# Performance work log

Hardware: AMD Instinct MI355X
Metric: run time of the kernel (lower is better)

Reference implementation:

```python
import jax, jax.numpy as jnp
import numpy as np

B, H, S, D = 4, 16, 2048, 64
SCALE_FACTOR = 8.0  # forward arg; module multiplies qk by 1/scale_factor = 0.125 = 1/sqrt(D)
# dropout_p is an undefined global in the source module; treated as 0 (identity)
# for a deterministic reference.

def setup_inputs() -> dict:
    key0 = jax.random.key(0)
    kq, kk, kv = jax.random.split(key0, 3)
    query = jax.random.normal(kq, (B, H, S, D), dtype=jnp.float32)
    key = jax.random.normal(kk, (B, H, S, D), dtype=jnp.float32)
    value = jax.random.normal(kv, (B, H, S, D), dtype=jnp.float32)
    return {"query": query, "key": key, "value": value}

def reference(query, key, value):
    inv_scale = 1.0 / SCALE_FACTOR
    # [B,H,S,S] attention scores (the module materializes this full matrix)
    qk = jnp.einsum('bhqd,bhkd->bhqk', query, key) * inv_scale
    probs = jax.nn.softmax(qk, axis=-1)
    # dropout is identity (p effectively 0 / eval-mode deterministic baseline)
    out = jnp.einsum('bhqk,bhkd->bhqd', probs, value)
    return out
```

## Files before the change

kernel.cpp:

```cpp
#include <hip/hip_runtime.h>
#include <hip/hip_bf16.h>

#define SEQ 2048
#define DIMH 64
#define KB 64
#define NT (SEQ / KB)

typedef __attribute__((ext_vector_type(8))) short bf16x8;
typedef __attribute__((ext_vector_type(4))) float f32x4;

extern "C" __device__ float __ocml_native_exp2_f32(float);
#define EXP2(x) __ocml_native_exp2_f32(x)

__device__ inline unsigned short f2bf(float f) {
    union { __bf16 h; unsigned short u; } c;
    c.h = (__bf16)f;
    return c.u;
}
__device__ inline unsigned pack2(float a, float b) {
    return (unsigned)f2bf(a) | ((unsigned)f2bf(b) << 16);
}

__device__ inline int swz(int row, int col) {
    int g = (((row & 7) ^ ((row >> 3) & 7)) << 3);
    return row * 64 + (col ^ g);
}

__device__ inline void perm32swap(unsigned &a, unsigned &b) {
    asm("v_permlane32_swap_b32 %0, %1" : "+v"(a), "+v"(b));
}
__device__ inline void perm16swap(unsigned &a, unsigned &b) {
    asm("v_permlane16_swap_b32 %0, %1" : "+v"(a), "+v"(b));
}

__global__ __launch_bounds__(256, 4) void fattn(
    const float* __restrict__ Q, const float* __restrict__ K,
    const float* __restrict__ V, float* __restrict__ O)
{
    __shared__ __align__(16) unsigned short Ksh[KB * DIMH];
    __shared__ __align__(16) unsigned short Vt[DIMH * KB];

    const int tid  = threadIdx.x;
    const int lane = tid & 63;
    const int wv   = tid >> 6;
    const int bh   = blockIdx.x >> 4;
    const int qt   = blockIdx.x & 15;

    const int l15 = lane & 15;
    const int lg  = lane >> 4;

    const float* qh = Q + (size_t)bh * SEQ * DIMH;
    const float* kh = K + (size_t)bh * SEQ * DIMH;
    const float* vh = V + (size_t)bh * SEQ * DIMH;
    float*       oh = O + (size_t)bh * SEQ * DIMH;

    const int q0 = qt * 128 + wv * 32;

    int koff[4][2];
    #pragma unroll
    for (int n = 0; n < 4; ++n)
        #pragma unroll
        for (int ks = 0; ks < 2; ++ks)
            koff[n][ks] = swz(n * 16 + l15, ks * 32 + lg * 8);

    const int c4 = (tid & 15) * 4;
    const int rK = tid >> 4;
    int kstoff[4], vstoff[4];
    #pragma unroll
    for (int rr = 0; rr < 4; ++rr) kstoff[rr] = swz(rr * 16 + rK, c4);
    #pragma unroll
    for (int j = 0; j < 4; ++j) vstoff[j] = swz(c4 + j, rK * 4);

    const float QS = 0.180336880111120f;
    bf16x8 qf[2][2];
    #pragma unroll
    for (int h = 0; h < 2; ++h)
        #pragma unroll
        for (int ks = 0; ks < 2; ++ks) {
            const float* src = qh + (size_t)(q0 + h * 16 + l15) * DIMH + ks * 32 + lg * 8;
            f32x4 a = *reinterpret_cast<const f32x4*>(src);
            f32x4 b = *reinterpret_cast<const f32x4*>(src + 4);
            bf16x8 vq;
            #pragma unroll
            for (int j = 0; j < 4; ++j) {
                vq[j]     = (short)f2bf(a[j] * QS);
                vq[j + 4] = (short)f2bf(b[j] * QS);
            }
            qf[h][ks] = vq;
        }

    bf16x8 ones;
    #pragma unroll
    for (int j = 0; j < 8; ++j) ones[j] = (short)0x3F80;

    f32x4 oacc[2][4];
    #pragma unroll
    for (int h = 0; h < 2; ++h)
        #pragma unroll
        for (int d = 0; d < 4; ++d) oacc[h][d] = (f32x4){0.f, 0.f, 0.f, 0.f};
    f32x4 lacc[2] = {{0.f,0.f,0.f,0.f}, {0.f,0.f,0.f,0.f}};

    for (int kt = 0; kt < NT; ++kt) {
        __syncthreads();

        #pragma unroll
        for (int rr = 0; rr < 4; ++rr) {
            const f32x4 k4 = *reinterpret_cast<const f32x4*>(
                kh + (size_t)(kt * KB + rr * 16 + rK) * DIMH + c4);
            uint2 kk;
            kk.x = pack2(k4[0], k4[1]);
            kk.y = pack2(k4[2], k4[3]);
            *reinterpret_cast<uint2*>(&Ksh[kstoff[rr]]) = kk;
        }
        {
            f32x4 v4[4];
            #pragma unroll
            for (int i = 0; i < 4; ++i)
                v4[i] = *reinterpret_cast<const f32x4*>(
                    vh + (size_t)(kt * KB + rK * 4 + i) * DIMH + c4);
            #pragma unroll
            for (int j = 0; j < 4; ++j) {
                uint2 w;
                w.x = pack2(v4[0][j], v4[1][j]);
                w.y = pack2(v4[2][j], v4[3][j]);
                *reinterpret_cast<uint2*>(&Vt[vstoff[j]]) = w;
            }
        }
        __syncthreads();

        __builtin_amdgcn_s_setprio(1);

        unsigned u[2][8];
        #pragma unroll
        for (int n = 0; n < 4; ++n) {
            bf16x8 kf0 = *reinterpret_cast<const bf16x8*>(&Ksh[koff[n][0]]);
            bf16x8 kf1 = *reinterpret_cast<const bf16x8*>(&Ksh[koff[n][1]]);
            #pragma unroll
            for (int h = 0; h < 2; ++h) {
                f32x4 a = {0.f, 0.f, 0.f, 0.f};
                a = __builtin_amdgcn_mfma_f32_16x16x32_bf16(kf0, qf[h][0], a, 0, 0, 0);
                a = __builtin_amdgcn_mfma_f32_16x16x32_bf16(kf1, qf[h][1], a, 0, 0, 0);
                u[h][2 * n]     = pack2(EXP2(a[0]), EXP2(a[1]));
                u[h][2 * n + 1] = pack2(EXP2(a[2]), EXP2(a[3]));
            }
        }

        bf16x8 pa[2][2];
        #pragma unroll
        for (int h = 0; h < 2; ++h)
            #pragma unroll
            for (int ks = 0; ks < 2; ++ks) {
                unsigned a0 = u[h][4 * ks + 0], b0 = u[h][4 * ks + 2];
                unsigned a1 = u[h][4 * ks + 1], b1 = u[h][4 * ks + 3];
                perm32swap(a0, b0); perm16swap(a0, b0);
                perm32swap(a1, b1); perm16swap(a1, b1);
                union { unsigned w[4]; bf16x8 v; } pu;
                pu.w[0] = a0; pu.w[1] = a1; pu.w[2] = b0; pu.w[3] = b1;
                pa[h][ks] = pu.v;
            }

        #pragma unroll
        for (int h = 0; h < 2; ++h) {
            lacc[h] = __builtin_amdgcn_mfma_f32_16x16x32_bf16(pa[h][0], ones, lacc[h], 0, 0, 0);
            lacc[h] = __builtin_amdgcn_mfma_f32_16x16x32_bf16(pa[h][1], ones, lacc[h], 0, 0, 0);
        }

        #pragma unroll
        for (int d = 0; d < 4; ++d) {
            bf16x8 vb0 = *reinterpret_cast<const bf16x8*>(&Vt[koff[d][0]]);
            bf16x8 vb1 = *reinterpret_cast<const bf16x8*>(&Vt[koff[d][1]]);
            #pragma unroll
            for (int h = 0; h < 2; ++h) {
                oacc[h][d] = __builtin_amdgcn_mfma_f32_16x16x32_bf16(pa[h][0], vb0, oacc[h][d], 0, 0, 0);
                oacc[h][d] = __builtin_amdgcn_mfma_f32_16x16x32_bf16(pa[h][1], vb1, oacc[h][d], 0, 0, 0);
            }
        }

        __builtin_amdgcn_s_setprio(0);
    }

    #pragma unroll
    for (int h = 0; h < 2; ++h)
        #pragma unroll
        for (int r = 0; r < 4; ++r) {
            float inv = 1.0f / lacc[h][r];
            float* dst = oh + (size_t)(q0 + h * 16 + lg * 4 + r) * DIMH;
            #pragma unroll
            for (int d = 0; d < 4; ++d)
                dst[d * 16 + l15] = oacc[h][d][r] * inv;
        }
}

extern "C" void kernel_launch(void* const* d_in, const int* in_sizes, int n_in,
                              void* d_out, int out_size, void* d_ws, size_t ws_size,
                              hipStream_t stream) {
    const float* q = (const float*)d_in[0];
    const float* k = (const float*)d_in[1];
    const float* v = (const float*)d_in[2];
    float* out = (float*)d_out;
    dim3 grid(64 * (SEQ / 128));
    dim3 block(256);
    fattn<<<grid, block, 0, stream>>>(q, k, v, out);
}
```

Baseline: 109.7 us.

## Double-buffer K/V tiles in LDS with register prefetch and remap block order

Splits the K and V shared-memory tiles into two buffers. The next tile's global loads are issued into registers before the P·V MFMAs of the current tile, then converted and stored into the other buffer afterwards, leaving one barrier per iteration instead of two. It also remaps block indices so that consecutive blocks map to different heads, changing L2 locality. The cost is 16 more KB of LDS and 32 extra VGPRs of prefetch registers, which may reduce occupancy under launch_bounds(256,4).

```diff
diff --git a/kernel.cpp b/kernel.cpp
--- a/kernel.cpp
+++ b/kernel.cpp
@@ -37,14 +37,17 @@
     const float* __restrict__ Q, const float* __restrict__ K,
     const float* __restrict__ V, float* __restrict__ O)
 {
-    __shared__ __align__(16) unsigned short Ksh[KB * DIMH];
-    __shared__ __align__(16) unsigned short Vt[DIMH * KB];
+    __shared__ __align__(16) unsigned short Ksh[2][KB * DIMH];
+    __shared__ __align__(16) unsigned short Vt[2][KB * DIMH];
 
     const int tid  = threadIdx.x;
     const int lane = tid & 63;
     const int wv   = tid >> 6;
-    const int bh   = blockIdx.x >> 4;
-    const int qt   = blockIdx.x & 15;
+
+    const int bid = blockIdx.x;
+    const int swb = (bid & 7) * 128 + (bid >> 3);
+    const int bh  = swb >> 4;
+    const int qt  = swb & 15;
 
     const int l15 = lane & 15;
     const int lg  = lane >> 4;
@@ -100,41 +103,43 @@
         for (int d = 0; d < 4; ++d) oacc[h][d] = (f32x4){0.f, 0.f, 0.f, 0.f};
     f32x4 lacc[2] = {{0.f,0.f,0.f,0.f}, {0.f,0.f,0.f,0.f}};
 
-    for (int kt = 0; kt < NT; ++kt) {
-        __syncthreads();
-
+    {
         #pragma unroll
         for (int rr = 0; rr < 4; ++rr) {
             const f32x4 k4 = *reinterpret_cast<const f32x4*>(
-                kh + (size_t)(kt * KB + rr * 16 + rK) * DIMH + c4);
+                kh + (size_t)(rr * 16 + rK) * DIMH + c4);
             uint2 kk;
             kk.x = pack2(k4[0], k4[1]);
             kk.y = pack2(k4[2], k4[3]);
-            *reinterpret_cast<uint2*>(&Ksh[kstoff[rr]]) = kk;
-        }
-        {
-            f32x4 v4[4];
-            #pragma unroll
-            for (int i = 0; i < 4; ++i)
-                v4[i] = *reinterpret_cast<const f32x4*>(
-                    vh + (size_t)(kt * KB + rK * 4 + i) * DIMH + c4);
-            #pragma unroll
-            for (int j = 0; j < 4; ++j) {
-                uint2 w;
-                w.x = pack2(v4[0][j], v4[1][j]);
-                w.y = pack2(v4[2][j], v4[3][j]);
-                *reinterpret_cast<uint2*>(&Vt[vstoff[j]]) = w;
-            }
-        }
-        __syncthreads();
+            *reinterpret_cast<uint2*>(&Ksh[0][kstoff[rr]]) = kk;
+        }
+        f32x4 v4[4];
+        #pragma unroll
+        for (int i = 0; i < 4; ++i)
+            v4[i] = *reinterpret_cast<const f32x4*>(
+                vh + (size_t)(rK * 4 + i) * DIMH + c4);
+        #pragma unroll
+        for (int j = 0; j < 4; ++j) {
+            uint2 w;
+            w.x = pack2(v4[0][j], v4[1][j]);
+            w.y = pack2(v4[2][j], v4[3][j]);
+            *reinterpret_cast<uint2*>(&Vt[0][vstoff[j]]) = w;
+        }
+    }
+    __syncthreads();
+
+    for (int kt = 0; kt < NT; ++kt) {
+        const int cur = kt & 1;
+        const unsigned short* Kb = Ksh[cur];
+        const unsigned short* Vb = Vt[cur];
 
         __builtin_amdgcn_s_setprio(1);
 
         unsigned u[2][8];
         #pragma unroll
         for (int n = 0; n < 4; ++n) {
-            bf16x8 kf0 = *reinterpret_cast<const bf16x8*>(&Ksh[koff[n][0]]);
-            bf16x8 kf1 = *reinterpret_cast<const bf16x8*>(&Ksh[koff[n][1]]);
+            bf16x8 kf0 = *reinterpret_cast<const bf16x8*>(&Kb[koff[n][0]]);
+            bf16x8 kf1 = *reinterpret_cast<const bf16x8*>(&Kb[koff[n][1]]);
             #pragma unroll
             for (int h = 0; h < 2; ++h) {
                 f32x4 a = {0.f, 0.f, 0.f, 0.f};
@@ -159,6 +164,20 @@
                 pa[h][ks] = pu.v;
             }
 
+        f32x4 kreg[4], vreg[4];
+        const bool pf = (kt + 1 < NT);
+        if (pf) {
+            const size_t tb = (size_t)(kt + 1) * KB;
+            #pragma unroll
+            for (int rr = 0; rr < 4; ++rr)
+                kreg[rr] = *reinterpret_cast<const f32x4*>(
+                    kh + (tb + rr * 16 + rK) * DIMH + c4);
+            #pragma unroll
+            for (int i = 0; i < 4; ++i)
+                vreg[i] = *reinterpret_cast<const f32x4*>(
+                    vh + (tb + rK * 4 + i) * DIMH + c4);
+        }
+
         #pragma unroll
         for (int h = 0; h < 2; ++h) {
             lacc[h] = __builtin_amdgcn_mfma_f32_16x16x32_bf16(pa[h][0], ones, lacc[h], 0, 0, 0);
@@ -167,8 +186,8 @@
 
         #pragma unroll
         for (int d = 0; d < 4; ++d) {
-            bf16x8 vb0 = *reinterpret_cast<const bf16x8*>(&Vt[koff[d][0]]);
-            bf16x8 vb1 = *reinterpret_cast<const bf16x8*>(&Vt[koff[d][1]]);
+            bf16x8 vb0 = *reinterpret_cast<const bf16x8*>(&Vb[koff[d][0]]);
+            bf16x8 vb1 = *reinterpret_cast<const bf16x8*>(&Vb[koff[d][1]]);
             #pragma unroll
             for (int h = 0; h < 2; ++h) {
                 oacc[h][d] = __builtin_amdgcn_mfma_f32_16x16x32_bf16(pa[h][0], vb0, oacc[h][d], 0, 0, 0);
@@ -177,6 +196,27 @@
         }
 
         __builtin_amdgcn_s_setprio(0);
+
+        if (pf) {
+            const int nxt = cur ^ 1;
+            #pragma unroll
+            for (int rr = 0; rr < 4; ++rr) {
+                uint2 kk;
+                kk.x = pack2(kreg[rr][0], kreg[rr][1]);
+                kk.y = pack2(kreg[rr][2], kreg[rr][3]);
+                *reinterpret_cast<uint2*>(&Ksh[nxt][kstoff[rr]]) = kk;
+            }
+            #pragma unroll
+            for (int j = 0; j < 4; ++j) {
+                uint2 w;
+                w.x = pack2(vreg[0][j], vreg[1][j]);
+                w.y = pack2(vreg[2][j], vreg[3][j]);
+                *reinterpret_cast<uint2*>(&Vt[nxt][vstoff[j]]) = w;
+            }
+            asm volatile("s_waitcnt lgkmcnt(0)" ::: "memory");
+            __builtin_amdgcn_s_barrier();
+            asm volatile("" ::: "memory");
+        }
     }
 
     #pragma unroll
```

Measured after the change: 113.3 us. 1.03x slower.
